# Kernel tuning notes

Measured on AMD Instinct MI355X. Metric: run time of the kernel, lower is better.

Reference implementation:

```python
import jax, jax.numpy as jnp
import numpy as np

B, S, D = 128, 256, 128
VOCAB, NH, K = 21, 4, 4
DI = 2 * D            # mLSTM inner dim (proj_factor=2)
QKB = 8               # qkv_proj_blocksize
NB = DI // QKB        # 32 block-diagonal qkv blocks
DHM = DI // NH        # 64 = mLSTM head dim
DHS = D // NH         # 32 = sLSTM head dim
FFU = 2 * D           # gated FFN up dim (proj_factor=2.0)


def _ln(x, w, eps=1e-5):
    mu = x.mean(-1, keepdims=True)
    var = x.var(-1, keepdims=True)
    return (x - mu) / jnp.sqrt(var + eps) * w


def _mh_ln(x, w, nh, eps=1e-5):
    # multi-head (group) layernorm: normalize each head's channels, scale by per-channel w
    b, s, d = x.shape
    xh = x.reshape(b, s, nh, d // nh)
    mu = xh.mean(-1, keepdims=True)
    var = xh.var(-1, keepdims=True)
    xn = (xh - mu) / jnp.sqrt(var + eps)
    return xn.reshape(b, s, d) * w


def _causal_conv(x, w, bias):
    # depthwise causal conv1d: x (B,S,C), w (C,K), left-pad K-1
    s = x.shape[1]
    k = w.shape[1]
    xp = jnp.pad(x, ((0, 0), (k - 1, 0), (0, 0)))
    return sum(xp[:, j:j + s, :] * w[:, j] for j in range(k)) + bias


def _blockdiag(x, w):
    # block-diagonal (headwise) linear: x (B,S,D), w (nb, out_per_block, in_per_block)
    b, s, d = x.shape
    nb = w.shape[0]
    xh = x.reshape(b, s, nb, d // nb)
    return jnp.einsum('bshd,hed->bshe', xh, w).reshape(b, s, -1)


def _mlstm_parallel(q, k, v, ip, fp, eps=1e-6):
    # parallel stabilized mLSTM; q,k,v (B,NH,S,DH); ip,fp (B,NH,S,1)
    b, nh, s, dh = q.shape
    log_f = jax.nn.log_sigmoid(fp)
    lf_cum = jnp.concatenate([jnp.zeros((b, nh, 1, 1), q.dtype),
                              jnp.cumsum(log_f, axis=2)], axis=2)      # (B,NH,S+1,1)
    m = lf_cum - jnp.swapaxes(lf_cum, -2, -1)                          # (B,NH,S+1,S+1)
    ltr = jnp.tril(jnp.ones((s, s), bool))
    log_fg = jnp.where(ltr, m[:, :, 1:, 1:], -jnp.inf)
    log_d = log_fg + jnp.swapaxes(ip, -2, -1)                          # (B,NH,S,S)
    max_d = jnp.max(log_d, axis=-1, keepdims=True)
    dmat = jnp.exp(log_d - max_d)
    qk = jnp.einsum('bhqd,bhkd->bhqk', q, k) / (dh ** 0.5)
    c = qk * dmat
    norm = jnp.maximum(jnp.abs(c.sum(-1, keepdims=True)), jnp.exp(-max_d))
    return jnp.einsum('bhqk,bhkd->bhqd', c / (norm + eps), v)


def _slstm_scan(gi, gf, gz, go, rec_w, bias):
    # sLSTM recurrence; g* (B,S,NH,DH); rec_w (NH,DH,4*DH); bias (NH,4*DH)
    b, s, nh, dh = gi.shape
    bi, bf, bz, bo = jnp.split(bias, 4, axis=-1)

    def step(carry, inp):
        h, c, n, m = carry
        ixt, fxt, zxt, oxt = inp
        rec = jnp.einsum('bhd,hde->bhe', h, rec_w)
        ri, rf, rz, ro = jnp.split(rec, 4, axis=-1)
        iraw = ixt + ri + bi
        fraw = fxt + rf + bf
        zraw = zxt + rz + bz
        oraw = oxt + ro + bo
        logfplusm = m + jax.nn.log_sigmoid(fraw)
        mnew = jnp.maximum(iraw, logfplusm)
        ig = jnp.exp(iraw - mnew)
        fg = jnp.exp(logfplusm - mnew)
        cnew = fg * c + ig * jnp.tanh(zraw)
        nnew = fg * n + ig
        hnew = jax.nn.sigmoid(oraw) * cnew / nnew
        return (hnew, cnew, nnew, mnew), hnew

    init = tuple(jnp.zeros((b, nh, dh), gi.dtype) for _ in range(4))
    xs = tuple(jnp.moveaxis(t, 1, 0) for t in (gi, gf, gz, go))
    _, ys = jax.lax.scan(step, init, xs)
    return jnp.moveaxis(ys, 0, 1)  # (B,S,NH,DH)


def _forward(x, emb, m_ln_w, m_up_w, m_conv_w, m_conv_b, m_q_w, m_k_w, m_v_w,
             m_ig_w, m_ig_b, m_fg_w, m_fg_b, m_on_w, m_skip, m_down_w,
             s_ln1_w, s_conv_w, s_conv_b, s_ig_w, s_fg_w, s_zg_w, s_og_w,
             s_rec_w, s_bias, s_gn_w, s_ln2_w, s_ff_up_w, s_ff_down_w,
             post_norm_w):
    h = emb[x]  # (B,S,D)
    # ---- block 0: mLSTM block (pre-LN residual) ----
    xn = _ln(h, m_ln_w)
    x_in, z = jnp.split(xn @ m_up_w.T, 2, axis=-1)          # each (B,S,DI)
    xca = jax.nn.silu(_causal_conv(x_in, m_conv_w, m_conv_b))
    q = _blockdiag(xca, m_q_w)
    kk = _blockdiag(xca, m_k_w)
    v = _blockdiag(x_in, m_v_w)
    ifin = jnp.concatenate([q, kk, v], axis=-1)             # (B,S,3*DI)
    ip = jnp.swapaxes(ifin @ m_ig_w.T + m_ig_b, 1, 2)[..., None]  # (B,NH,S,1)
    fp = jnp.swapaxes(ifin @ m_fg_w.T + m_fg_b, 1, 2)[..., None]
    to_heads = lambda t: jnp.swapaxes(t.reshape(B, S, NH, DHM), 1, 2)
    ht = _mlstm_parallel(to_heads(q), to_heads(kk), to_heads(v), ip, fp)
    hm = jnp.swapaxes(ht, 1, 2).reshape(B, S, DI)
    hm = _mh_ln(hm, m_on_w, NH)
    hm = (hm + m_skip * xca) * jax.nn.silu(z)
    h = h + hm @ m_down_w.T
    # ---- blocks 1,2: sLSTM blocks (pre-LN residual + gated gelu FFN) ----
    for i in range(2):
        xn = _ln(h, s_ln1_w[i])
        xc = jax.nn.silu(_causal_conv(xn, s_conv_w[i], s_conv_b[i]))
        gi = _blockdiag(xc, s_ig_w[i]).reshape(B, S, NH, DHS)
        gf = _blockdiag(xc, s_fg_w[i]).reshape(B, S, NH, DHS)
        gz = _blockdiag(xn, s_zg_w[i]).reshape(B, S, NH, DHS)
        go = _blockdiag(xn, s_og_w[i]).reshape(B, S, NH, DHS)
        y = _slstm_scan(gi, gf, gz, go, s_rec_w[i], s_bias[i])
        h = h + _mh_ln(y.reshape(B, S, D), s_gn_w[i], NH)
        xn2 = _ln(h, s_ln2_w[i])
        gate, up = jnp.split(xn2 @ s_ff_up_w[i].T, 2, axis=-1)
        h = h + (jax.nn.gelu(gate, approximate=False) * up) @ s_ff_down_w[i].T
    return _ln(h, post_norm_w)


def setup_inputs():
    key = jax.random.key(0)
    ks = iter(jax.random.split(key, 64))
    r = lambda shape, s=0.02: jax.random.normal(next(ks), shape, jnp.float32) * s
    inp = {}
    inp['x'] = jax.random.randint(next(ks), (B, S), 0, VOCAB)
    inp['emb'] = r((VOCAB, D)).at[0].set(0.0)  # padding_idx=0
    inp['m_ln_w'] = jnp.ones((D,), jnp.float32)
    inp['m_up_w'] = r((2 * DI, D))
    inp['m_conv_w'] = r((DI, K), 0.1)
    inp['m_conv_b'] = jnp.zeros((DI,), jnp.float32)
    inp['m_q_w'] = r((NB, QKB, QKB), 0.1)
    inp['m_k_w'] = r((NB, QKB, QKB), 0.1)
    inp['m_v_w'] = r((NB, QKB, QKB), 0.1)
    inp['m_ig_w'] = r((NH, 3 * DI))
    inp['m_ig_b'] = r((NH,), 0.1)
    inp['m_fg_w'] = r((NH, 3 * DI))
    inp['m_fg_b'] = jnp.linspace(3.0, 6.0, NH)  # forget-gate bias init
    inp['m_on_w'] = jnp.ones((DI,), jnp.float32)
    inp['m_skip'] = jnp.ones((DI,), jnp.float32)
    inp['m_down_w'] = r((D, DI))
    inp['s_ln1_w'] = jnp.ones((2, D), jnp.float32)
    inp['s_conv_w'] = r((2, D, K), 0.1)
    inp['s_conv_b'] = jnp.zeros((2, D), jnp.float32)
    inp['s_ig_w'] = r((2, NH, DHS, DHS), 0.05)
    inp['s_fg_w'] = r((2, NH, DHS, DHS), 0.05)
    inp['s_zg_w'] = r((2, NH, DHS, DHS), 0.05)
    inp['s_og_w'] = r((2, NH, DHS, DHS), 0.05)
    inp['s_rec_w'] = r((2, NH, DHS, 4 * DHS), 0.05)
    inp['s_bias'] = jnp.zeros((2, NH, 4 * DHS), jnp.float32).at[:, :, DHS:2 * DHS].set(jnp.linspace(3.0, 6.0, DHS))
    inp['s_gn_w'] = jnp.ones((2, D), jnp.float32)
    inp['s_ln2_w'] = jnp.ones((2, D), jnp.float32)
    inp['s_ff_up_w'] = r((2, 2 * FFU, D))
    inp['s_ff_down_w'] = r((2, D, FFU))
    inp['post_norm_w'] = jnp.ones((D,), jnp.float32)
    return inp


def reference(x, emb, m_ln_w, m_up_w, m_conv_w, m_conv_b, m_q_w, m_k_w, m_v_w,
              m_ig_w, m_ig_b, m_fg_w, m_fg_b, m_on_w, m_skip, m_down_w,
              s_ln1_w, s_conv_w, s_conv_b, s_ig_w, s_fg_w, s_zg_w, s_og_w,
              s_rec_w, s_bias, s_gn_w, s_ln2_w, s_ff_up_w, s_ff_down_w,
              post_norm_w):
    return _forward(x, emb, m_ln_w, m_up_w, m_conv_w, m_conv_b, m_q_w, m_k_w, m_v_w,
                    m_ig_w, m_ig_b, m_fg_w, m_fg_b, m_on_w, m_skip, m_down_w,
                    s_ln1_w, s_conv_w, s_conv_b, s_ig_w, s_fg_w, s_zg_w, s_og_w,
                    s_rec_w, s_bias, s_gn_w, s_ln2_w, s_ff_up_w, s_ff_down_w,
                    post_norm_w)
```

## Files before the change

### kernel.cpp

```cpp
#include <hip/hip_runtime.h>
#include <hip/hip_bf16.h>

#define BB 128
#define SS 256
#define DD 128
#define DI 256
#define NH 4
#define DHM 64
#define DHS 32
#define NROWS (BB*SS)

#define WAVE_SYNC() do { asm volatile("s_waitcnt lgkmcnt(0)" ::: "memory"); __builtin_amdgcn_wave_barrier(); } while (0)

typedef __attribute__((ext_vector_type(8))) short short8;
typedef __attribute__((ext_vector_type(4))) float f32x4;
typedef __attribute__((ext_vector_type(2))) int i32x2;

__device__ __forceinline__ float sigmoidf_(float x) { return 1.f / (1.f + __expf(-x)); }
__device__ __forceinline__ float siluf_(float x) { return x / (1.f + __expf(-x)); }
__device__ __forceinline__ float logsigf_(float x) {
    return (x >= 0.f) ? -log1pf(__expf(-x)) : x - log1pf(__expf(x));
}
__device__ __forceinline__ float geluf_(float g) {
    return 0.5f * g * (1.f + erff(g * 0.70710678118654752f));
}
__device__ __forceinline__ ushort bf16u(float x) {
    unsigned u = __float_as_uint(x);
    u += 0x7fffu + ((u >> 16) & 1u);
    return (ushort)(u >> 16);
}
__device__ __forceinline__ float ubf(ushort v) {
    return __uint_as_float((unsigned)v << 16);
}
__device__ __forceinline__ float rdlane(float v, int lane) {
    return __int_as_float(__builtin_amdgcn_readlane(__float_as_int(v), lane));
}
#define DPPADD(x, ctrl) ((x) + __int_as_float(__builtin_amdgcn_update_dpp(0, __float_as_int(x), (ctrl), 0xf, 0xf, true)))

__global__ __launch_bounds__(256) void tobf16_kernel(const float* __restrict__ src,
        ushort* __restrict__ dst, int n) {
    int i = blockIdx.x * 256 + threadIdx.x;
    if (i < n) dst[i] = bf16u(src[i]);
}

__global__ __launch_bounds__(256) void densify_kernel(const float* __restrict__ wi,
        const float* __restrict__ wf, const float* __restrict__ wz,
        const float* __restrict__ wo, ushort* __restrict__ dst) {
    int idx = blockIdx.x * 256 + threadIdx.x;
    int t = idx & 127;
    int oc = (idx >> 7) & 255;
    int pair = (idx >> 15) & 1;
    int i2 = idx >> 16;
    int h = oc >> 6, l = oc & 63, gate = (l >> 5) & 1, e = l & 31;
    const float* w = pair == 0 ? (gate == 0 ? wi : wf) : (gate == 0 ? wz : wo);
    float val = ((t >> 5) == h) ? w[i2 * 4096 + h * 1024 + e * 32 + (t & 31)] : 0.f;
    dst[idx] = bf16u(val);
}

__global__ __launch_bounds__(256) void densify_mgate_kernel(const float* __restrict__ igw,
        const float* __restrict__ fgw, ushort* __restrict__ dst) {
    int idx = blockIdx.x * 256 + threadIdx.x;
    if (idx >= 16 * 768) return;
    int t = idx % 768, j = idx / 768;
    float v = 0.f;
    if (j < 4) v = igw[j * 768 + t];
    else if (j < 8) v = fgw[(j - 4) * 768 + t];
    dst[idx] = bf16u(v);
}

__global__ __launch_bounds__(256) void embed_kernel(const int* __restrict__ x,
        const float* __restrict__ emb, float* __restrict__ h, int total) {
    int i = blockIdx.x * 256 + threadIdx.x;
    if (i >= total) return;
    int row = i >> 7;
    int c = i & 127;
    h[i] = emb[x[row] * DD + c];
}

__global__ __launch_bounds__(256) void ln128_kernel(const float* __restrict__ x,
        const float* __restrict__ w, float* __restrict__ out, ushort* __restrict__ outb) {
    int row = blockIdx.x * 4 + (threadIdx.x >> 6);
    int lane = threadIdx.x & 63;
    const float* xr = x + (size_t)row * DD;
    float a = xr[lane], b = xr[lane + 64];
    float s1 = a + b, s2 = a * a + b * b;
    #pragma unroll
    for (int o = 32; o; o >>= 1) { s1 += __shfl_xor(s1, o); s2 += __shfl_xor(s2, o); }
    float mu = s1 * (1.f / 128.f);
    float var = s2 * (1.f / 128.f) - mu * mu;
    float inv = rsqrtf(var + 1e-5f);
    float va = (a - mu) * inv * w[lane];
    float vb = (b - mu) * inv * w[lane + 64];
    if (out) {
        float* orow = out + (size_t)row * DD;
        orow[lane] = va; orow[lane + 64] = vb;
    }
    ushort* brow = outb + (size_t)row * DD;
    brow[lane] = bf16u(va); brow[lane + 64] = bf16u(vb);
}

__global__ __launch_bounds__(256, 2) void gemm_bf16_kernel(const ushort* __restrict__ A, int lda,
        const ushort* __restrict__ W, float* __restrict__ C, ushort* __restrict__ Cb,
        int ldc, int K, int addC) {
    __shared__ ushort As[128 * 32];
    __shared__ ushort Bs[128 * 32];
    int m0 = blockIdx.x * 128;
    int n0 = blockIdx.y * 128;
    int tid = threadIdx.x;
    int wv = tid >> 6, l = tid & 63;
    int lr = l & 15, lg = l >> 4, g4 = lg * 4;
    int wr = wv >> 1, wc = wv & 1;
    int sr = tid >> 1;
    int sc = (tid & 1) * 2;

    f32x4 acc[4][4] = {};
    for (int k0 = 0; k0 < K; k0 += 32) {
        __syncthreads();
        #pragma unroll
        for (int u = 0; u < 2; ++u) {
            int c = sc + u;
            uint4 av = *(const uint4*)(A + (size_t)(m0 + sr) * lda + k0 + c * 8);
            *(uint4*)(As + sr * 32 + ((c ^ (sr & 3)) * 8)) = av;
            uint4 wv4 = *(const uint4*)(W + (size_t)(n0 + sr) * K + k0 + c * 8);
            *(uint4*)(Bs + sr * 32 + ((c ^ (sr & 3)) * 8)) = wv4;
        }
        __syncthreads();
        short8 af[4], bf[4];
        #pragma unroll
        for (int fm = 0; fm < 4; ++fm) {
            int row = wr * 64 + fm * 16 + lr;
            af[fm] = *(const short8*)(As + row * 32 + ((lg ^ (row & 3)) * 8));
        }
        #pragma unroll
        for (int fn = 0; fn < 4; ++fn) {
            int row = wc * 64 + fn * 16 + lr;
            bf[fn] = *(const short8*)(Bs + row * 32 + ((lg ^ (row & 3)) * 8));
        }
        #pragma unroll
        for (int fm = 0; fm < 4; ++fm)
            #pragma unroll
            for (int fn = 0; fn < 4; ++fn)
                acc[fm][fn] = __builtin_amdgcn_mfma_f32_16x16x32_bf16(af[fm], bf[fn], acc[fm][fn], 0, 0, 0);
    }
    #pragma unroll
    for (int fm = 0; fm < 4; ++fm) {
        #pragma unroll
        for (int fn = 0; fn < 4; ++fn) {
            #pragma unroll
            for (int r = 0; r < 4; ++r) {
                size_t idx = (size_t)(m0 + wr * 64 + fm * 16 + g4 + r) * ldc + n0 + wc * 64 + fn * 16 + lr;
                if (Cb) Cb[idx] = bf16u(acc[fm][fn][r]);
                else if (addC) C[idx] += acc[fm][fn][r];
                else C[idx] = acc[fm][fn][r];
            }
        }
    }
}

__global__ __launch_bounds__(256, 2) void gemm_glu_kernel(const ushort* __restrict__ xzb,
        const ushort* __restrict__ W, float* __restrict__ C) {
    __shared__ ushort As[128 * 32];
    __shared__ ushort Bs[128 * 32];
    int m0 = blockIdx.x * 128;
    int tid = threadIdx.x;
    int wv = tid >> 6, l = tid & 63;
    int lr = l & 15, lg = l >> 4, g4 = lg * 4;
    int wr = wv >> 1, wc = wv & 1;
    int sr = tid >> 1;
    int sc = (tid & 1) * 2;

    f32x4 acc[4][4] = {};
    for (int k0 = 0; k0 < 256; k0 += 32) {
        __syncthreads();
        #pragma unroll
        for (int u = 0; u < 2; ++u) {
            int c = sc + u;
            short8 g8 = *(const short8*)(xzb + (size_t)(m0 + sr) * 512 + k0 + c * 8);
            short8 u8 = *(const short8*)(xzb + (size_t)(m0 + sr) * 512 + 256 + k0 + c * 8);
            short8 o8;
            #pragma unroll
            for (int t = 0; t < 8; ++t)
                o8[t] = (short)bf16u(geluf_(ubf((ushort)g8[t])) * ubf((ushort)u8[t]));
            *(short8*)(As + sr * 32 + ((c ^ (sr & 3)) * 8)) = o8;
            uint4 wv4 = *(const uint4*)(W + (size_t)sr * 256 + k0 + c * 8);
            *(uint4*)(Bs + sr * 32 + ((c ^ (sr & 3)) * 8)) = wv4;
        }
        __syncthreads();
        short8 af[4], bf[4];
        #pragma unroll
        for (int fm = 0; fm < 4; ++fm) {
            int row = wr * 64 + fm * 16 + lr;
            af[fm] = *(const short8*)(As + row * 32 + ((lg ^ (row & 3)) * 8));
        }
        #pragma unroll
        for (int fn = 0; fn < 4; ++fn) {
            int row = wc * 64 + fn * 16 + lr;
            bf[fn] = *(const short8*)(Bs + row * 32 + ((lg ^ (row & 3)) * 8));
        }
        #pragma unroll
        for (int fm = 0; fm < 4; ++fm)
            #pragma unroll
            for (int fn = 0; fn < 4; ++fn)
                acc[fm][fn] = __builtin_amdgcn_mfma_f32_16x16x32_bf16(af[fm], bf[fn], acc[fm][fn], 0, 0, 0);
    }
    #pragma unroll
    for (int fm = 0; fm < 4; ++fm) {
        #pragma unroll
        for (int fn = 0; fn < 4; ++fn) {
            #pragma unroll
            for (int r = 0; r < 4; ++r) {
                size_t idx = (size_t)(m0 + wr * 64 + fm * 16 + g4 + r) * 128 + wc * 64 + fn * 16 + lr;
                C[idx] += acc[fm][fn][r];
            }
        }
    }
}

__global__ __launch_bounds__(256) void gategemm_kernel(const ushort* __restrict__ qb,
        const ushort* __restrict__ kb, const ushort* __restrict__ vb,
        const ushort* __restrict__ W16, const float* __restrict__ igb,
        const float* __restrict__ fgb, float* __restrict__ ip, float* __restrict__ fp) {
    int tid = threadIdx.x;
    int wv = tid >> 6, l = tid & 63;
    int lr = l & 15, lg = l >> 4, g4 = lg * 4;
    int row0 = blockIdx.x * 128 + wv * 32;
    f32x4 acc[2] = {};
    #pragma unroll
    for (int k0 = 0; k0 < 768; k0 += 32) {
        short8 bfr = *(const short8*)(W16 + lr * 768 + k0 + lg * 8);
        #pragma unroll
        for (int mi = 0; mi < 2; ++mi) {
            int row = row0 + mi * 16 + lr;
            int b = row >> 8, s = row & 255;
            const ushort* src;
            size_t addr;
            if (k0 < 256) {
                src = qb;
                addr = ((size_t)(b * 4 + (k0 >> 6)) * 256 + s) * 64 + (k0 & 63) + lg * 8;
            } else if (k0 < 512) {
                int kq = k0 - 256;
                src = kb;
                addr = ((size_t)(b * 4 + (kq >> 6)) * 256 + s) * 64 + (kq & 63) + lg * 8;
            } else {
                src = vb;
                addr = (size_t)row * 256 + (k0 - 512) + lg * 8;
            }
            short8 afr = *(const short8*)(src + addr);
            acc[mi] = __builtin_amdgcn_mfma_f32_16x16x32_bf16(afr, bfr, acc[mi], 0, 0, 0);
        }
    }
    if (lr < 8) {
        float bias = (lr < 4) ? igb[lr] : fgb[lr - 4];
        float* dst = (lr < 4) ? ip : fp;
        int hh = lr & 3;
        #pragma unroll
        for (int mi = 0; mi < 2; ++mi) {
            #pragma unroll
            for (int r = 0; r < 4; ++r) {
                int row = row0 + mi * 16 + g4 + r;
                int b = row >> 8, s = row & 255;
                dst[(size_t)(b * 4 + hh) * 256 + s] = acc[mi][r] + bias;
            }
        }
    }
}

__global__ __launch_bounds__(256) void conv_silu_s_kernel(const ushort* __restrict__ xb,
        const float* __restrict__ w, const float* __restrict__ bias,
        ushort* __restrict__ outb, int total) {
    int i = blockIdx.x * 256 + threadIdx.x;
    if (i >= total) return;
    int c = i & 127;
    size_t row = (size_t)(i >> 7);
    int s = (int)(row & (SS - 1));
    float acc = bias[c];
    #pragma unroll
    for (int j = 0; j < 4; ++j) {
        int ss = s - 3 + j;
        if (ss >= 0) acc += ubf(xb[(row + (size_t)(j - 3)) * 128 + c]) * w[c * 4 + j];
    }
    outb[i] = bf16u(siluf_(acc));
}

__global__ __launch_bounds__(256) void mqkv_kernel(const ushort* __restrict__ xzb,
        const float* __restrict__ cw, const float* __restrict__ cb,
        const float* __restrict__ qw, const float* __restrict__ kw,
        const float* __restrict__ vw, ushort* __restrict__ xcab,
        ushort* __restrict__ qb16, ushort* __restrict__ kb16,
        ushort* __restrict__ vb16, int total) {
    int i = blockIdx.x * 256 + threadIdx.x;
    if (i >= total) return;
    int c = i & 255;
    size_t row = (size_t)(i >> 8);
    int nb = c >> 3, e = c & 7;
    int s = (int)(row & (SS - 1));
    float xin[4][8];
    #pragma unroll
    for (int j = 0; j < 4; ++j) {
        int ss = s - 3 + j;
        if (ss >= 0) {
            short8 v8 = *(const short8*)(xzb + (row + (size_t)(j - 3)) * 512 + nb * 8);
            #pragma unroll
            for (int t = 0; t < 8; ++t) xin[j][t] = ubf((ushort)v8[t]);
        } else {
            #pragma unroll
            for (int t = 0; t < 8; ++t) xin[j][t] = 0.f;
        }
    }
    float xc8[8];
    #pragma unroll
    for (int t = 0; t < 8; ++t) {
        int ch = nb * 8 + t;
        float acc = cb[ch];
        #pragma unroll
        for (int j = 0; j < 4; ++j) acc += xin[j][t] * cw[ch * 4 + j];
        xc8[t] = siluf_(acc);
    }
    const float* qw8 = qw + (size_t)(nb * 8 + e) * 8;
    const float* kw8 = kw + (size_t)(nb * 8 + e) * 8;
    const float* vw8 = vw + (size_t)(nb * 8 + e) * 8;
    float aq = 0.f, ak = 0.f, av = 0.f;
    #pragma unroll
    for (int t = 0; t < 8; ++t) {
        aq += xc8[t] * qw8[t];
        ak += xc8[t] * kw8[t];
        av += xin[3][t] * vw8[t];
    }
    xcab[row * 256 + c] = bf16u(xc8[e]);
    vb16[row * 256 + c] = bf16u(av);
    int h2 = c >> 6, dd = c & 63;
    size_t be = ((((row >> 8) << 2) + h2) * 256 + (row & 255)) * 64 + dd;
    qb16[be] = bf16u(aq);
    kb16[be] = bf16u(ak);
}

__global__ __launch_bounds__(64) void mprep_kernel(const float* __restrict__ ip,
        const float* __restrict__ fp, float* __restrict__ L,
        float* __restrict__ E, float* __restrict__ PM) {
    int bh = blockIdx.x;
    int lane = threadIdx.x;
    size_t base = (size_t)bh * SS + lane * 4;
    float lsv[4], ipv[4];
    #pragma unroll
    for (int u = 0; u < 4; ++u) {
        lsv[u] = logsigf_(fp[base + u]);
        ipv[u] = ip[base + u];
    }
    float p0 = lsv[0], p1 = p0 + lsv[1], p2 = p1 + lsv[2], p3 = p2 + lsv[3];
    float inc = p3;
    #pragma unroll
    for (int o = 1; o < 64; o <<= 1) {
        float wv = __shfl_up(inc, o);
        if (lane >= o) inc += wv;
    }
    float excl = inc - p3;
    float Lv[4] = {excl + p0, excl + p1, excl + p2, excl + p3};
    float Ev[4];
    #pragma unroll
    for (int u = 0; u < 4; ++u) Ev[u] = ipv[u] - Lv[u];
    float q0 = Ev[0], q1 = fmaxf(q0, Ev[1]), q2 = fmaxf(q1, Ev[2]), q3 = fmaxf(q2, Ev[3]);
    float incm = q3;
    #pragma unroll
    for (int o = 1; o < 64; o <<= 1) {
        float wv = __shfl_up(incm, o);
        if (lane >= o) incm = fmaxf(incm, wv);
    }
    float exm = __shfl_up(incm, 1);
    if (lane == 0) exm = -INFINITY;
    float qv[4] = {q0, q1, q2, q3};
    #pragma unroll
    for (int u = 0; u < 4; ++u) {
        L[base + u] = Lv[u];
        E[base + u] = Ev[u];
        PM[base + u] = fmaxf(exm, qv[u]);
    }
}

__global__ __launch_bounds__(256) void vtrans_kernel(const ushort* __restrict__ vb,
        ushort* __restrict__ vt) {
    int blk = blockIdx.x;
    int st = blk & 3, bh = blk >> 2;
    int b = bh >> 2, h = bh & 3;
    int tid = threadIdx.x;
    __shared__ ushort tile[64][68];
    int s0 = st * 64;
    #pragma unroll
    for (int u = 0; u < 16; ++u) {
        int idx = u * 256 + tid;
        int sl = idx >> 6, dl = idx & 63;
        tile[sl][dl] = vb[((size_t)(b * 256 + s0 + sl)) * 256 + h * 64 + dl];
    }
    __syncthreads();
    #pragma unroll
    for (int u = 0; u < 16; ++u) {
        int idx = u * 256 + tid;
        int dl = idx >> 6, sl = idx & 63;
        vt[((size_t)bh * 64 + dl) * 256 + s0 + sl] = tile[sl][dl];
    }
}

__global__ __launch_bounds__(256, 2) void mlstm_mfma_kernel(
        const ushort* __restrict__ qb, const ushort* __restrict__ kb,
        const ushort* __restrict__ vt, const float* __restrict__ Lg,
        const float* __restrict__ Eg, const float* __restrict__ PMg,
        float* __restrict__ hmout) {
    int bh = blockIdx.x;
    int b = bh >> 2, h = bh & 3;
    int tid = threadIdx.x;
    int wv = tid >> 6, l = tid & 63;
    int lr = l & 15, lg = l >> 4, g4 = lg * 4;

    __shared__ ushort Kb[16384];
    __shared__ ushort Vt[16384];
    __shared__ ushort Pl[4 * 640];
    __shared__ float sE[SS], sPM[SS], sL[SS];

    const size_t gb16 = (size_t)bh * 16384;
    #pragma unroll
    for (int p2 = 0; p2 < 8; ++p2) {
        int id = p2 * 256 + tid;
        int r = id >> 3, c = id & 7;
        uint4 kval = *(const uint4*)(kb + gb16 + r * 64 + c * 8);
        *(uint4*)(Kb + r * 64 + ((c ^ (r & 7)) * 8)) = kval;
        int d = id >> 5, c2 = id & 31;
        uint4 vval = *(const uint4*)(vt + gb16 + d * 256 + c2 * 8);
        *(uint4*)(Vt + d * 256 + ((c2 ^ (d & 7)) * 8)) = vval;
    }
    sE[tid]  = Eg[(size_t)bh * SS + tid];
    sPM[tid] = PMg[(size_t)bh * SS + tid];
    sL[tid]  = Lg[(size_t)bh * SS + tid];
    __syncthreads();

    f32x4 O[4][4] = {};
    float csum[4][4] = {};
    const int pmap[4] = {wv, 7 - wv, 8 + wv, 15 - wv};
    ushort* Pw = Pl + wv * 640;
    size_t obase = (size_t)(b * SS) * 256 + h * 64;

    #pragma unroll
    for (int rf = 0; rf < 4; ++rf) {
        int p = pmap[rf];
        int r0 = p * 16;
        short8 qf0 = *(const short8*)(qb + gb16 + (r0 + lr) * 64 + lg * 8);
        short8 qf1 = *(const short8*)(qb + gb16 + (r0 + lr) * 64 + 32 + lg * 8);
        float pmv[4], lv[4];
        #pragma unroll
        for (int r = 0; r < 4; ++r) { pmv[r] = sPM[r0 + g4 + r]; lv[r] = sL[r0 + g4 + r]; }
        int jtmax = r0 >> 5;
        #pragma unroll 1
        for (int jt = 0; jt <= jtmax; ++jt) {
            int jb = jt * 32;
            f32x4 s0 = {0.f, 0.f, 0.f, 0.f}, s1 = {0.f, 0.f, 0.f, 0.f};
            {
                int j = jb + lr;
                int sw = j & 7;
                short8 k00 = *(const short8*)(Kb + j * 64 + ((lg)     ^ sw) * 8);
                short8 k01 = *(const short8*)(Kb + j * 64 + ((4 + lg) ^ sw) * 8);
                int j2 = jb + 16 + lr;
                int sw2 = j2 & 7;
                short8 k10 = *(const short8*)(Kb + j2 * 64 + ((lg)     ^ sw2) * 8);
                short8 k11 = *(const short8*)(Kb + j2 * 64 + ((4 + lg) ^ sw2) * 8);
                s0 = __builtin_amdgcn_mfma_f32_16x16x32_bf16(qf0, k00, s0, 0, 0, 0);
                s0 = __builtin_amdgcn_mfma_f32_16x16x32_bf16(qf1, k01, s0, 0, 0, 0);
                s1 = __builtin_amdgcn_mfma_f32_16x16x32_bf16(qf0, k10, s1, 0, 0, 0);
                s1 = __builtin_amdgcn_mfma_f32_16x16x32_bf16(qf1, k11, s1, 0, 0, 0);
            }
            float e0 = sE[jb + lr], e1 = sE[jb + 16 + lr];
            int j0 = jb + lr, j1 = jb + 16 + lr;
            #pragma unroll
            for (int r = 0; r < 4; ++r) {
                int i = r0 + g4 + r;
                float sc0 = (j0 <= i) ? s0[r] * 0.125f * __expf(e0 - pmv[r]) : 0.f;
                float sc1 = (j1 <= i) ? s1[r] * 0.125f * __expf(e1 - pmv[r]) : 0.f;
                csum[rf][r] += sc0 + sc1;
                Pw[(g4 + r) * 40 + lr] = bf16u(sc0);
                Pw[(g4 + r) * 40 + 16 + lr] = bf16u(sc1);
            }
            WAVE_SYNC();
            short8 pf = *(const short8*)(Pw + lr * 40 + lg * 8);
            #pragma unroll
            for (int dc = 0; dc < 4; ++dc) {
                int d = dc * 16 + lr;
                int chunk = (jt * 4 + lg) ^ (d & 7);
                short8 vf = *(const short8*)(Vt + d * 256 + chunk * 8);
                O[rf][dc] = __builtin_amdgcn_mfma_f32_16x16x32_bf16(pf, vf, O[rf][dc], 0, 0, 0);
            }
        }
        float rinv[4];
        #pragma unroll
        for (int r = 0; r < 4; ++r) {
            float cs = csum[rf][r];
            cs += __shfl_xor(cs, 1); cs += __shfl_xor(cs, 2);
            cs += __shfl_xor(cs, 4); cs += __shfl_xor(cs, 8);
            float nrm = fmaxf(fabsf(cs), __expf(-(lv[r] + pmv[r]))) + 1e-6f;
            rinv[r] = 1.f / nrm;
        }
        #pragma unroll
        for (int dc = 0; dc < 4; ++dc)
            #pragma unroll
            for (int r = 0; r < 4; ++r)
                hmout[obase + (size_t)(r0 + g4 + r) * 256 + dc * 16 + lr] = O[rf][dc][r] * rinv[r];
    }
}

__global__ __launch_bounds__(256) void mpost_kernel(const float* __restrict__ hm,
        const ushort* __restrict__ xzb, const ushort* __restrict__ xcab,
        const float* __restrict__ onw, const float* __restrict__ skip,
        ushort* __restrict__ outb) {
    int row = blockIdx.x;
    int t = threadIdx.x;
    float hv = hm[(size_t)row * 256 + t];
    float s1 = hv, s2 = hv * hv;
    #pragma unroll
    for (int o = 32; o; o >>= 1) { s1 += __shfl_xor(s1, o); s2 += __shfl_xor(s2, o); }
    float mu = s1 * (1.f / 64.f);
    float var = s2 * (1.f / 64.f) - mu * mu;
    float xnv = (hv - mu) * rsqrtf(var + 1e-5f) * onw[t];
    float z = ubf(xzb[(size_t)row * 512 + 256 + t]);
    float val = (xnv + skip[t] * ubf(xcab[(size_t)row * 256 + t])) * siluf_(z);
    outb[(size_t)row * 256 + t] = bf16u(val);
}

__global__ __launch_bounds__(64, 1) void slstm_scan_kernel(const ushort* __restrict__ gifb,
        const ushort* __restrict__ gzob, const float* __restrict__ rec_w,
        const float* __restrict__ bias, const float* __restrict__ gnw,
        float* __restrict__ hbuf) {
    int bh = blockIdx.x;
    int b = bh >> 2, h = bh & 3;
    int l = threadIdx.x;
    int c = l & 31;
    bool lo = (l < 32);
    unsigned wpk[32];
    const float* wp = rec_w + (size_t)h * 4096 + l;
    #pragma unroll
    for (int d = 0; d < 32; ++d) {
        float w0v = wp[d * 128];
        float w1v = wp[d * 128 + 64];
        wpk[d] = ((unsigned)bf16u(w1v) << 16) | (unsigned)bf16u(w0v);
    }
    float b0 = bias[h * 128 + l];
    float b1 = bias[h * 128 + 64 + l];
    float gw = gnw[h * 32 + c];
    float cst = 0.f, nst = 0.f, hreg = 0.f;
    size_t gb = (size_t)b * SS * 256 + h * 64 + l;
    size_t hb = (size_t)b * SS * 128 + h * 32 + c;
    float pg0[4], pg1[4], ph[4];
    #pragma unroll
    for (int u = 0; u < 4; ++u) {
        pg0[u] = ubf(gifb[gb + (size_t)u * 256]);
        pg1[u] = ubf(gzob[gb + (size_t)u * 256]);
        ph[u]  = hbuf[hb + (size_t)u * 128];
    }
    for (int s = 0; s < SS; s += 4) {
        #pragma unroll
        for (int u = 0; u < 4; ++u) {
            float a00 = 0.f, a01 = 0.f, a02 = 0.f, a03 = 0.f;
            float a10 = 0.f, a11 = 0.f, a12 = 0.f, a13 = 0.f;
            #pragma unroll
            for (int d = 0; d < 32; d += 4) {
                float h0 = rdlane(hreg, d);
                float h1 = rdlane(hreg, d + 1);
                float h2 = rdlane(hreg, d + 2);
                float h3 = rdlane(hreg, d + 3);
                unsigned p0 = wpk[d], p1 = wpk[d + 1], p2 = wpk[d + 2], p3 = wpk[d + 3];
                a00 += __uint_as_float(p0 << 16) * h0;
                a10 += __uint_as_float(p0) * h0;
                a01 += __uint_as_float(p1 << 16) * h1;
                a11 += __uint_as_float(p1) * h1;
                a02 += __uint_as_float(p2 << 16) * h2;
                a12 += __uint_as_float(p2) * h2;
                a03 += __uint_as_float(p3 << 16) * h3;
                a13 += __uint_as_float(p3) * h3;
            }
            float raw0 = pg0[u] + ((a00 + a01) + (a02 + a03)) + b0;
            float raw1 = pg1[u] + ((a10 + a11) + (a12 + a13)) + b1;
            float hcur = ph[u];
            int s4 = s + 4 + u;
            if (s4 < SS) {
                pg0[u] = ubf(gifb[gb + (size_t)s4 * 256]);
                pg1[u] = ubf(gzob[gb + (size_t)s4 * 256]);
                ph[u]  = hbuf[hb + (size_t)s4 * 128];
            }
            i32x2 r0p = __builtin_amdgcn_permlane32_swap(__float_as_int(raw0), __float_as_int(raw0), false, false);
            i32x2 r1p = __builtin_amdgcn_permlane32_swap(__float_as_int(raw1), __float_as_int(raw1), false, false);
            float q0 = __int_as_float(lo ? r0p.y : r0p.x);
            float q1 = __int_as_float(lo ? r1p.y : r1p.x);
            float iraw = lo ? raw0 : q0;
            float zraw = lo ? raw1 : q1;
            float fraw = lo ? q0 : raw0;
            float oraw = lo ? q1 : raw1;
            float fg = __builtin_amdgcn_rcpf(1.f + __expf(-fraw));
            float ig = __expf(iraw);
            float e2z = __expf(2.f * zraw);
            float tz = 1.f - 2.f * __builtin_amdgcn_rcpf(e2z + 1.f);
            cst = fg * cst + ig * tz;
            nst = fg * nst + ig;
            float sg = __builtin_amdgcn_rcpf(1.f + __expf(-oraw));
            float hv = sg * cst * __builtin_amdgcn_rcpf(nst);
            hreg = hv;
            float s1 = hv, s2 = hv * hv;
            s1 = DPPADD(s1, 0x111); s2 = DPPADD(s2, 0x111);
            s1 = DPPADD(s1, 0x112); s2 = DPPADD(s2, 0x112);
            s1 = DPPADD(s1, 0x114); s2 = DPPADD(s2, 0x114);
            s1 = DPPADD(s1, 0x118); s2 = DPPADD(s2, 0x118);
            s1 = DPPADD(s1, 0x142); s2 = DPPADD(s2, 0x142);
            s1 = DPPADD(s1, 0x143); s2 = DPPADD(s2, 0x143);
            float mu = rdlane(s1, 63) * (1.f / 64.f);
            float var = rdlane(s2, 63) * (1.f / 64.f) - mu * mu;
            float outv = (hv - mu) * rsqrtf(var + 1e-5f) * gw;
            if (lo) hbuf[hb + (size_t)(s + u) * 128] = hcur + outv;
        }
    }
}

extern "C" void kernel_launch(void* const* d_in, const int* in_sizes, int n_in,
                              void* d_out, int out_size, void* d_ws, size_t ws_size,
                              hipStream_t stream) {
    const int*   x        = (const int*)d_in[0];
    const float* emb      = (const float*)d_in[1];
    const float* m_ln_w   = (const float*)d_in[2];
    const float* m_up_w   = (const float*)d_in[3];
    const float* m_conv_w = (const float*)d_in[4];
    const float* m_conv_b = (const float*)d_in[5];
    const float* m_q_w    = (const float*)d_in[6];
    const float* m_k_w    = (const float*)d_in[7];
    const float* m_v_w    = (const float*)d_in[8];
    const float* m_ig_w   = (const float*)d_in[9];
    const float* m_ig_b   = (const float*)d_in[10];
    const float* m_fg_w   = (const float*)d_in[11];
    const float* m_fg_b   = (const float*)d_in[12];
    const float* m_on_w   = (const float*)d_in[13];
    const float* m_skip   = (const float*)d_in[14];
    const float* m_down_w = (const float*)d_in[15];
    const float* s_ln1_w  = (const float*)d_in[16];
    const float* s_conv_w = (const float*)d_in[17];
    const float* s_conv_b = (const float*)d_in[18];
    const float* s_ig_w   = (const float*)d_in[19];
    const float* s_fg_w   = (const float*)d_in[20];
    const float* s_zg_w   = (const float*)d_in[21];
    const float* s_og_w   = (const float*)d_in[22];
    const float* s_rec_w  = (const float*)d_in[23];
    const float* s_bias   = (const float*)d_in[24];
    const float* s_gn_w   = (const float*)d_in[25];
    const float* s_ln2_w  = (const float*)d_in[26];
    const float* s_ff_up_w   = (const float*)d_in[27];
    const float* s_ff_down_w = (const float*)d_in[28];
    const float* post_norm_w = (const float*)d_in[29];
    float* out = (float*)d_out;

    float* ws = (float*)d_ws;
    const size_t NR = NROWS;
    float* h   = ws;
    float* hm  = h   + NR * 128;
    float* regA = hm  + NR * 256;
    float* regB = regA + NR * 128;
    float* gip = regB + NR * 128;
    float* gfp = gip + 512 * 256;
    float* gL  = gfp + 512 * 256;
    float* gE  = gL  + 512 * 256;
    float* gPM = gE  + 512 * 256;
    float* extra = gPM + 512 * 256;
    ushort* xnb   = (ushort*)extra;
    ushort* xzb   = xnb + NR * 128;
    ushort* xcab  = xzb + NR * 512;
    ushort* qb16  = xcab + NR * 256;
    ushort* vb16  = qb16 + NR * 256;
    ushort* upb   = vb16 + NR * 256;
    ushort* downb = upb + 512 * 128;
    ushort* ffupb = downb + 128 * 256;
    ushort* ffdownb = ffupb + 2 * 512 * 128;
    ushort* sgwb  = ffdownb + 2 * 128 * 256;
    ushort* w16b  = sgwb + 2 * 2 * 256 * 128;
    ushort* kb16   = (ushort*)out;
    ushort* vtb    = (ushort*)regA;
    ushort* gifb   = (ushort*)regA;
    ushort* mpostb = (ushort*)regB;
    ushort* gzob   = (ushort*)regB;
    ushort* xcb    = qb16;

    tobf16_kernel<<<(512 * 128 + 255) / 256, 256, 0, stream>>>(m_up_w, upb, 512 * 128);
    tobf16_kernel<<<(128 * 256 + 255) / 256, 256, 0, stream>>>(m_down_w, downb, 128 * 256);
    tobf16_kernel<<<(2 * 512 * 128 + 255) / 256, 256, 0, stream>>>(s_ff_up_w, ffupb, 2 * 512 * 128);
    tobf16_kernel<<<(2 * 128 * 256 + 255) / 256, 256, 0, stream>>>(s_ff_down_w, ffdownb, 2 * 128 * 256);
    densify_kernel<<<(2 * 2 * 256 * 128) / 256, 256, 0, stream>>>(s_ig_w, s_fg_w, s_zg_w, s_og_w, sgwb);
    densify_mgate_kernel<<<(16 * 768 + 255) / 256, 256, 0, stream>>>(m_ig_w, m_fg_w, w16b);

    embed_kernel<<<(NR * 128) / 256, 256, 0, stream>>>(x, emb, h, NR * 128);
    ln128_kernel<<<NR / 4, 256, 0, stream>>>(h, m_ln_w, nullptr, xnb);
    gemm_bf16_kernel<<<dim3(NR / 128, 4), 256, 0, stream>>>(xnb, 128, upb, nullptr, xzb, 512, 128, 0);
    mqkv_kernel<<<(NR * 256) / 256, 256, 0, stream>>>(xzb, m_conv_w, m_conv_b,
            m_q_w, m_k_w, m_v_w, xcab, qb16, kb16, vb16, NR * 256);
    gategemm_kernel<<<NR / 128, 256, 0, stream>>>(qb16, kb16, vb16, w16b, m_ig_b, m_fg_b, gip, gfp);
    mprep_kernel<<<BB * NH, 64, 0, stream>>>(gip, gfp, gL, gE, gPM);
    vtrans_kernel<<<BB * NH * 4, 256, 0, stream>>>(vb16, vtb);
    mlstm_mfma_kernel<<<BB * NH, 256, 0, stream>>>(qb16, kb16, vtb, gL, gE, gPM, hm);
    mpost_kernel<<<NR, 256, 0, stream>>>(hm, xzb, xcab, m_on_w, m_skip, mpostb);
    gemm_bf16_kernel<<<dim3(NR / 128, 1), 256, 0, stream>>>(mpostb, 256, downb, h, nullptr, 128, 256, 1);

    for (int i2 = 0; i2 < 2; ++i2) {
        ln128_kernel<<<NR / 4, 256, 0, stream>>>(h, s_ln1_w + i2 * 128, nullptr, xnb);
        conv_silu_s_kernel<<<(NR * 128) / 256, 256, 0, stream>>>(xnb, s_conv_w + i2 * 128 * 4,
                s_conv_b + i2 * 128, xcb, NR * 128);
        gemm_bf16_kernel<<<dim3(NR / 128, 2), 256, 0, stream>>>(xcb, 128, sgwb + (size_t)(i2 * 2 + 0) * 256 * 128, nullptr, gifb, 256, 128, 0);
        gemm_bf16_kernel<<<dim3(NR / 128, 2), 256, 0, stream>>>(xnb, 128, sgwb + (size_t)(i2 * 2 + 1) * 256 * 128, nullptr, gzob, 256, 128, 0);
        slstm_scan_kernel<<<BB * NH, 64, 0, stream>>>(gifb, gzob,
                s_rec_w + i2 * 4 * 32 * 128, s_bias + i2 * 4 * 128, s_gn_w + i2 * 128, h);
        ln128_kernel<<<NR / 4, 256, 0, stream>>>(h, s_ln2_w + i2 * 128, nullptr, xnb);
        gemm_bf16_kernel<<<dim3(NR / 128, 4), 256, 0, stream>>>(xnb, 128, ffupb + (size_t)i2 * 512 * 128, nullptr, xzb, 512, 128, 0);
        gemm_glu_kernel<<<NR / 128, 256, 0, stream>>>(xzb, ffdownb + (size_t)i2 * 128 * 256, h);
    }
    ln128_kernel<<<NR / 4, 256, 0, stream>>>(h, post_norm_w, out, xnb);
}
```

Baseline: 726.7 us.

## Fuse weight prep, embed+LN, mLSTM post-norm, sLSTM gate GEMMs, defer scan norm

Six weight-conversion launches are merged into one kernel, and embedding lookup is fused with the first layernorm. The mLSTM output normalization, skip and gating are folded into the attention kernel, so the fp32 hm buffer no longer round-trips through memory. The two sLSTM gate GEMMs become one launch, and the sLSTM scan defers each step's group-norm reduction and store into the next step to overlap it with the recurrence. The final layernorm no longer writes an unused bf16 copy. The mLSTM epilogue now issues strided, less coalesced bf16 loads and stores from inside the attention kernel.

```diff
diff --git a/kernel.cpp b/kernel.cpp
--- a/kernel.cpp
+++ b/kernel.cpp
@@ -37,44 +37,65 @@
 }
 #define DPPADD(x, ctrl) ((x) + __int_as_float(__builtin_amdgcn_update_dpp(0, __float_as_int(x), (ctrl), 0xf, 0xf, true)))
 
-__global__ __launch_bounds__(256) void tobf16_kernel(const float* __restrict__ src,
-        ushort* __restrict__ dst, int n) {
-    int i = blockIdx.x * 256 + threadIdx.x;
-    if (i < n) dst[i] = bf16u(src[i]);
-}
-
-__global__ __launch_bounds__(256) void densify_kernel(const float* __restrict__ wi,
+__global__ __launch_bounds__(256) void wprep_kernel(const float* __restrict__ m_up_w,
+        const float* __restrict__ m_down_w, const float* __restrict__ s_ff_up_w,
+        const float* __restrict__ s_ff_down_w, const float* __restrict__ wi,
         const float* __restrict__ wf, const float* __restrict__ wz,
-        const float* __restrict__ wo, ushort* __restrict__ dst) {
-    int idx = blockIdx.x * 256 + threadIdx.x;
-    int t = idx & 127;
-    int oc = (idx >> 7) & 255;
-    int pair = (idx >> 15) & 1;
-    int i2 = idx >> 16;
-    int h = oc >> 6, l = oc & 63, gate = (l >> 5) & 1, e = l & 31;
-    const float* w = pair == 0 ? (gate == 0 ? wi : wf) : (gate == 0 ? wz : wo);
-    float val = ((t >> 5) == h) ? w[i2 * 4096 + h * 1024 + e * 32 + (t & 31)] : 0.f;
-    dst[idx] = bf16u(val);
-}
-
-__global__ __launch_bounds__(256) void densify_mgate_kernel(const float* __restrict__ igw,
-        const float* __restrict__ fgw, ushort* __restrict__ dst) {
-    int idx = blockIdx.x * 256 + threadIdx.x;
-    if (idx >= 16 * 768) return;
-    int t = idx % 768, j = idx / 768;
-    float v = 0.f;
-    if (j < 4) v = igw[j * 768 + t];
-    else if (j < 8) v = fgw[(j - 4) * 768 + t];
-    dst[idx] = bf16u(v);
-}
-
-__global__ __launch_bounds__(256) void embed_kernel(const int* __restrict__ x,
-        const float* __restrict__ emb, float* __restrict__ h, int total) {
-    int i = blockIdx.x * 256 + threadIdx.x;
-    if (i >= total) return;
-    int row = i >> 7;
-    int c = i & 127;
-    h[i] = emb[x[row] * DD + c];
+        const float* __restrict__ wo, const float* __restrict__ igw,
+        const float* __restrict__ fgw,
+        ushort* __restrict__ upb, ushort* __restrict__ downb,
+        ushort* __restrict__ ffupb, ushort* __restrict__ ffdownb,
+        ushort* __restrict__ sgwb, ushort* __restrict__ w16b) {
+    int gid = blockIdx.x * 256 + threadIdx.x;
+    if (gid < 65536) {
+        upb[gid] = bf16u(m_up_w[gid]);
+    } else if (gid < 98304) {
+        int i = gid - 65536;
+        downb[i] = bf16u(m_down_w[i]);
+    } else if (gid < 229376) {
+        int i = gid - 98304;
+        ffupb[i] = bf16u(s_ff_up_w[i]);
+    } else if (gid < 294912) {
+        int i = gid - 229376;
+        ffdownb[i] = bf16u(s_ff_down_w[i]);
+    } else if (gid < 557056) {
+        int idx = gid - 294912;
+        int t = idx & 127;
+        int oc = (idx >> 7) & 255;
+        int pair = (idx >> 15) & 1;
+        int i2 = idx >> 16;
+        int h = oc >> 6, l = oc & 63, gate = (l >> 5) & 1, e = l & 31;
+        const float* w = pair == 0 ? (gate == 0 ? wi : wf) : (gate == 0 ? wz : wo);
+        float val = ((t >> 5) == h) ? w[i2 * 4096 + h * 1024 + e * 32 + (t & 31)] : 0.f;
+        sgwb[idx] = bf16u(val);
+    } else if (gid < 569344) {
+        int idx = gid - 557056;
+        int t = idx % 768, j = idx / 768;
+        float v = 0.f;
+        if (j < 4) v = igw[j * 768 + t];
+        else if (j < 8) v = fgw[(j - 4) * 768 + t];
+        w16b[idx] = bf16u(v);
+    }
+}
+
+__global__ __launch_bounds__(256) void embed_ln_kernel(const int* __restrict__ x,
+        const float* __restrict__ emb, const float* __restrict__ w,
+        float* __restrict__ h, ushort* __restrict__ outb) {
+    int row = blockIdx.x * 4 + (threadIdx.x >> 6);
+    int lane = threadIdx.x & 63;
+    int tok = x[row];
+    float a = emb[tok * DD + lane], b = emb[tok * DD + 64 + lane];
+    h[(size_t)row * DD + lane] = a;
+    h[(size_t)row * DD + 64 + lane] = b;
+    float s1 = a + b, s2 = a * a + b * b;
+    #pragma unroll
+    for (int o = 32; o; o >>= 1) { s1 += __shfl_xor(s1, o); s2 += __shfl_xor(s2, o); }
+    float mu = s1 * (1.f / 128.f);
+    float var = s2 * (1.f / 128.f) - mu * mu;
+    float inv = rsqrtf(var + 1e-5f);
+    ushort* brow = outb + (size_t)row * DD;
+    brow[lane] = bf16u((a - mu) * inv * w[lane]);
+    brow[lane + 64] = bf16u((b - mu) * inv * w[lane + 64]);
 }
 
 __global__ __launch_bounds__(256) void ln128_kernel(const float* __restrict__ x,
@@ -95,8 +116,10 @@
         float* orow = out + (size_t)row * DD;
         orow[lane] = va; orow[lane + 64] = vb;
     }
-    ushort* brow = outb + (size_t)row * DD;
-    brow[lane] = bf16u(va); brow[lane + 64] = bf16u(vb);
+    if (outb) {
+        ushort* brow = outb + (size_t)row * DD;
+        brow[lane] = bf16u(va); brow[lane + 64] = bf16u(vb);
+    }
 }
 
 __global__ __launch_bounds__(256, 2) void gemm_bf16_kernel(const ushort* __restrict__ A, int lda,
@@ -157,6 +180,64 @@
     }
 }
 
+__global__ __launch_bounds__(256, 2) void sgate_gemm_kernel(const ushort* __restrict__ xcb,
+        const ushort* __restrict__ xnb, const ushort* __restrict__ Wif,
+        const ushort* __restrict__ Wzo, ushort* __restrict__ gifb, ushort* __restrict__ gzob) {
+    __shared__ ushort As[128 * 32];
+    __shared__ ushort Bs[128 * 32];
+    int y = blockIdx.y;
+    const ushort* A = (y < 2) ? xcb : xnb;
+    const ushort* W = (y < 2) ? Wif : Wzo;
+    ushort* Cb = (y < 2) ? gifb : gzob;
+    int m0 = blockIdx.x * 128;
+    int n0 = (y & 1) * 128;
+    int tid = threadIdx.x;
+    int wv = tid >> 6, l = tid & 63;
+    int lr = l & 15, lg = l >> 4, g4 = lg * 4;
+    int wr = wv >> 1, wc = wv & 1;
+    int sr = tid >> 1;
+    int sc = (tid & 1) * 2;
+
+    f32x4 acc[4][4] = {};
+    for (int k0 = 0; k0 < 128; k0 += 32) {
+        __syncthreads();
+        #pragma unroll
+        for (int u = 0; u < 2; ++u) {
+            int c = sc + u;
+            uint4 av = *(const uint4*)(A + (size_t)(m0 + sr) * 128 + k0 + c * 8);
+            *(uint4*)(As + sr * 32 + ((c ^ (sr & 3)) * 8)) = av;
+            uint4 wv4 = *(const uint4*)(W + (size_t)(n0 + sr) * 128 + k0 + c * 8);
+            *(uint4*)(Bs + sr * 32 + ((c ^ (sr & 3)) * 8)) = wv4;
+        }
+        __syncthreads();
+        short8 af[4], bf[4];
+        #pragma unroll
+        for (int fm = 0; fm < 4; ++fm) {
+            int row = wr * 64 + fm * 16 + lr;
+            af[fm] = *(const short8*)(As + row * 32 + ((lg ^ (row & 3)) * 8));
+        }
+        #pragma unroll
+        for (int fn = 0; fn < 4; ++fn) {
+            int row = wc * 64 + fn * 16 + lr;
+            bf[fn] = *(const short8*)(Bs + row * 32 + ((lg ^ (row & 3)) * 8));
+        }
+        #pragma unroll
+        for (int fm = 0; fm < 4; ++fm)
+            #pragma unroll
+            for (int fn = 0; fn < 4; ++fn)
+                acc[fm][fn] = __builtin_amdgcn_mfma_f32_16x16x32_bf16(af[fm], bf[fn], acc[fm][fn], 0, 0, 0);
+    }
+    #pragma unroll
+    for (int fm = 0; fm < 4; ++fm)
+        #pragma unroll
+        for (int fn = 0; fn < 4; ++fn)
+            #pragma unroll
+            for (int r = 0; r < 4; ++r) {
+                size_t idx = (size_t)(m0 + wr * 64 + fm * 16 + g4 + r) * 256 + n0 + wc * 64 + fn * 16 + lr;
+                Cb[idx] = bf16u(acc[fm][fn][r]);
+            }
+}
+
 __global__ __launch_bounds__(256, 2) void gemm_glu_kernel(const ushort* __restrict__ xzb,
         const ushort* __restrict__ W, float* __restrict__ C) {
     __shared__ ushort As[128 * 32];
@@ -204,16 +285,14 @@
                 acc[fm][fn] = __builtin_amdgcn_mfma_f32_16x16x32_bf16(af[fm], bf[fn], acc[fm][fn], 0, 0, 0);
     }
     #pragma unroll
-    for (int fm = 0; fm < 4; ++fm) {
-        #pragma unroll
-        for (int fn = 0; fn < 4; ++fn) {
+    for (int fm = 0; fm < 4; ++fm)
+        #pragma unroll
+        for (int fn = 0; fn < 4; ++fn)
             #pragma unroll
             for (int r = 0; r < 4; ++r) {
                 size_t idx = (size_t)(m0 + wr * 64 + fm * 16 + g4 + r) * 128 + wc * 64 + fn * 16 + lr;
                 C[idx] += acc[fm][fn][r];
             }
-        }
-    }
 }
 
 __global__ __launch_bounds__(256) void gategemm_kernel(const ushort* __restrict__ qb,
@@ -403,7 +482,9 @@
         const ushort* __restrict__ qb, const ushort* __restrict__ kb,
         const ushort* __restrict__ vt, const float* __restrict__ Lg,
         const float* __restrict__ Eg, const float* __restrict__ PMg,
-        float* __restrict__ hmout) {
+        const ushort* __restrict__ xzb, const ushort* __restrict__ xcab,
+        const float* __restrict__ onw, const float* __restrict__ skip,
+        ushort* __restrict__ outb) {
     int bh = blockIdx.x;
     int b = bh >> 2, h = bh & 3;
     int tid = threadIdx.x;
@@ -431,11 +512,18 @@
     sL[tid]  = Lg[(size_t)bh * SS + tid];
     __syncthreads();
 
+    float onwv[4], skipv[4];
+    #pragma unroll
+    for (int dc = 0; dc < 4; ++dc) {
+        int ch = h * 64 + dc * 16 + lr;
+        onwv[dc] = onw[ch];
+        skipv[dc] = skip[ch];
+    }
+
     f32x4 O[4][4] = {};
     float csum[4][4] = {};
     const int pmap[4] = {wv, 7 - wv, 8 + wv, 15 - wv};
     ushort* Pw = Pl + wv * 640;
-    size_t obase = (size_t)(b * SS) * 256 + h * 64;
 
     #pragma unroll
     for (int rf = 0; rf < 4; ++rf) {
@@ -486,39 +574,36 @@
                 O[rf][dc] = __builtin_amdgcn_mfma_f32_16x16x32_bf16(pf, vf, O[rf][dc], 0, 0, 0);
             }
         }
-        float rinv[4];
         #pragma unroll
         for (int r = 0; r < 4; ++r) {
             float cs = csum[rf][r];
             cs += __shfl_xor(cs, 1); cs += __shfl_xor(cs, 2);
             cs += __shfl_xor(cs, 4); cs += __shfl_xor(cs, 8);
             float nrm = fmaxf(fabsf(cs), __expf(-(lv[r] + pmv[r]))) + 1e-6f;
-            rinv[r] = 1.f / nrm;
-        }
-        #pragma unroll
-        for (int dc = 0; dc < 4; ++dc)
-            #pragma unroll
-            for (int r = 0; r < 4; ++r)
-                hmout[obase + (size_t)(r0 + g4 + r) * 256 + dc * 16 + lr] = O[rf][dc][r] * rinv[r];
-    }
-}
-
-__global__ __launch_bounds__(256) void mpost_kernel(const float* __restrict__ hm,
-        const ushort* __restrict__ xzb, const ushort* __restrict__ xcab,
-        const float* __restrict__ onw, const float* __restrict__ skip,
-        ushort* __restrict__ outb) {
-    int row = blockIdx.x;
-    int t = threadIdx.x;
-    float hv = hm[(size_t)row * 256 + t];
-    float s1 = hv, s2 = hv * hv;
-    #pragma unroll
-    for (int o = 32; o; o >>= 1) { s1 += __shfl_xor(s1, o); s2 += __shfl_xor(s2, o); }
-    float mu = s1 * (1.f / 64.f);
-    float var = s2 * (1.f / 64.f) - mu * mu;
-    float xnv = (hv - mu) * rsqrtf(var + 1e-5f) * onw[t];
-    float z = ubf(xzb[(size_t)row * 512 + 256 + t]);
-    float val = (xnv + skip[t] * ubf(xcab[(size_t)row * 256 + t])) * siluf_(z);
-    outb[(size_t)row * 256 + t] = bf16u(val);
+            float rinv = 1.f / nrm;
+            float v0 = O[rf][0][r] * rinv, v1 = O[rf][1][r] * rinv;
+            float v2 = O[rf][2][r] * rinv, v3 = O[rf][3][r] * rinv;
+            float s1m = v0 + v1 + v2 + v3;
+            float s2m = v0 * v0 + v1 * v1 + v2 * v2 + v3 * v3;
+            s1m += __shfl_xor(s1m, 1); s2m += __shfl_xor(s2m, 1);
+            s1m += __shfl_xor(s1m, 2); s2m += __shfl_xor(s2m, 2);
+            s1m += __shfl_xor(s1m, 4); s2m += __shfl_xor(s2m, 4);
+            s1m += __shfl_xor(s1m, 8); s2m += __shfl_xor(s2m, 8);
+            float mu = s1m * (1.f / 64.f);
+            float var = s2m * (1.f / 64.f) - mu * mu;
+            float inv = rsqrtf(var + 1e-5f);
+            int grow = b * 256 + r0 + g4 + r;
+            float vv[4] = {v0, v1, v2, v3};
+            #pragma unroll
+            for (int dc = 0; dc < 4; ++dc) {
+                int ch = h * 64 + dc * 16 + lr;
+                float z = ubf(xzb[(size_t)grow * 512 + 256 + ch]);
+                float xnv = (vv[dc] - mu) * inv * onwv[dc];
+                float val = (xnv + skipv[dc] * ubf(xcab[(size_t)grow * 256 + ch])) * siluf_(z);
+                outb[(size_t)grow * 256 + ch] = bf16u(val);
+            }
+        }
+    }
 }
 
 __global__ __launch_bounds__(64, 1) void slstm_scan_kernel(const ushort* __restrict__ gifb,
@@ -551,6 +636,8 @@
         pg1[u] = ubf(gzob[gb + (size_t)u * 256]);
         ph[u]  = hbuf[hb + (size_t)u * 128];
     }
+    float pend_hv = 0.f, pend_hcur = 0.f;
+    int pend_off = 0;
     for (int s = 0; s < SS; s += 4) {
         #pragma unroll
         for (int u = 0; u < 4; ++u) {
@@ -575,6 +662,19 @@
             float raw0 = pg0[u] + ((a00 + a01) + (a02 + a03)) + b0;
             float raw1 = pg1[u] + ((a10 + a11) + (a12 + a13)) + b1;
             float hcur = ph[u];
+            {
+                float s1 = pend_hv, s2 = pend_hv * pend_hv;
+                s1 = DPPADD(s1, 0x111); s2 = DPPADD(s2, 0x111);
+                s1 = DPPADD(s1, 0x112); s2 = DPPADD(s2, 0x112);
+                s1 = DPPADD(s1, 0x114); s2 = DPPADD(s2, 0x114);
+                s1 = DPPADD(s1, 0x118); s2 = DPPADD(s2, 0x118);
+                s1 = DPPADD(s1, 0x142); s2 = DPPADD(s2, 0x142);
+                s1 = DPPADD(s1, 0x143); s2 = DPPADD(s2, 0x143);
+                float mu = rdlane(s1, 63) * (1.f / 64.f);
+                float var = rdlane(s2, 63) * (1.f / 64.f) - mu * mu;
+                float outv = (pend_hv - mu) * rsqrtf(var + 1e-5f) * gw;
+                if (lo) hbuf[hb + (size_t)pend_off * 128] = pend_hcur + outv;
+            }
             int s4 = s + 4 + u;
             if (s4 < SS) {
                 pg0[u] = ubf(gifb[gb + (size_t)s4 * 256]);
@@ -598,18 +698,23 @@
             float sg = __builtin_amdgcn_rcpf(1.f + __expf(-oraw));
             float hv = sg * cst * __builtin_amdgcn_rcpf(nst);
             hreg = hv;
-            float s1 = hv, s2 = hv * hv;
-            s1 = DPPADD(s1, 0x111); s2 = DPPADD(s2, 0x111);
-            s1 = DPPADD(s1, 0x112); s2 = DPPADD(s2, 0x112);
-            s1 = DPPADD(s1, 0x114); s2 = DPPADD(s2, 0x114);
-            s1 = DPPADD(s1, 0x118); s2 = DPPADD(s2, 0x118);
-            s1 = DPPADD(s1, 0x142); s2 = DPPADD(s2, 0x142);
-            s1 = DPPADD(s1, 0x143); s2 = DPPADD(s2, 0x143);
-            float mu = rdlane(s1, 63) * (1.f / 64.f);
-            float var = rdlane(s2, 63) * (1.f / 64.f) - mu * mu;
-            float outv = (hv - mu) * rsqrtf(var + 1e-5f) * gw;
-            if (lo) hbuf[hb + (size_t)(s + u) * 128] = hcur + outv;
-        }
+            pend_hv = hv;
+            pend_hcur = hcur;
+            pend_off = s + u;
+        }
+    }
+    {
+        float s1 = pend_hv, s2 = pend_hv * pend_hv;
+        s1 = DPPADD(s1, 0x111); s2 = DPPADD(s2, 0x111);
+        s1 = DPPADD(s1, 0x112); s2 = DPPADD(s2, 0x112);
+        s1 = DPPADD(s1, 0x114); s2 = DPPADD(s2, 0x114);
+        s1 = DPPADD(s1, 0x118); s2 = DPPADD(s2, 0x118);
+        s1 = DPPADD(s1, 0x142); s2 = DPPADD(s2, 0x142);
+        s1 = DPPADD(s1, 0x143); s2 = DPPADD(s2, 0x143);
+        float mu = rdlane(s1, 63) * (1.f / 64.f);
+        float var = rdlane(s2, 63) * (1.f / 64.f) - mu * mu;
+        float outv = (pend_hv - mu) * rsqrtf(var + 1e-5f) * gw;
+        if (lo) hbuf[hb + (size_t)pend_off * 128] = pend_hcur + outv;
     }
 }
 
@@ -651,8 +756,7 @@
     float* ws = (float*)d_ws;
     const size_t NR = NROWS;
     float* h   = ws;
-    float* hm  = h   + NR * 128;
-    float* regA = hm  + NR * 256;
+    float* regA = h   + NR * 128;
     float* regB = regA + NR * 128;
     float* gip = regB + NR * 128;
     float* gfp = gip + 512 * 256;
@@ -678,36 +782,33 @@
     ushort* gzob   = (ushort*)regB;
     ushort* xcb    = qb16;
 
-    tobf16_kernel<<<(512 * 128 + 255) / 256, 256, 0, stream>>>(m_up_w, upb, 512 * 128);
-    tobf16_kernel<<<(128 * 256 + 255) / 256, 256, 0, stream>>>(m_down_w, downb, 128 * 256);
-    tobf16_kernel<<<(2 * 512 * 128 + 255) / 256, 256, 0, stream>>>(s_ff_up_w, ffupb, 2 * 512 * 128);
-    tobf16_kernel<<<(2 * 128 * 256 + 255) / 256, 256, 0, stream>>>(s_ff_down_w, ffdownb, 2 * 128 * 256);
-    densify_kernel<<<(2 * 2 * 256 * 128) / 256, 256, 0, stream>>>(s_ig_w, s_fg_w, s_zg_w, s_og_w, sgwb);
-    densify_mgate_kernel<<<(16 * 768 + 255) / 256, 256, 0, stream>>>(m_ig_w, m_fg_w, w16b);
-
-    embed_kernel<<<(NR * 128) / 256, 256, 0, stream>>>(x, emb, h, NR * 128);
-    ln128_kernel<<<NR / 4, 256, 0, stream>>>(h, m_ln_w, nullptr, xnb);
+    wprep_kernel<<<(569344 + 255) / 256, 256, 0, stream>>>(m_up_w, m_down_w, s_ff_up_w,
+            s_ff_down_w, s_ig_w, s_fg_w, s_zg_w, s_og_w, m_ig_w, m_fg_w,
+            upb, downb, ffupb, ffdownb, sgwb, w16b);
+
+    embed_ln_kernel<<<NR / 4, 256, 0, stream>>>(x, emb, m_ln_w, h, xnb);
     gemm_bf16_kernel<<<dim3(NR / 128, 4), 256, 0, stream>>>(xnb, 128, upb, nullptr, xzb, 512, 128, 0);
     mqkv_kernel<<<(NR * 256) / 256, 256, 0, stream>>>(xzb, m_conv_w, m_conv_b,
             m_q_w, m_k_w, m_v_w, xcab, qb16, kb16, vb16, NR * 256);
     gategemm_kernel<<<NR / 128, 256, 0, stream>>>(qb16, kb16, vb16, w16b, m_ig_b, m_fg_b, gip, gfp);
     mprep_kernel<<<BB * NH, 64, 0, stream>>>(gip, gfp, gL, gE, gPM);
     vtrans_kernel<<<BB * NH * 4, 256, 0, stream>>>(vb16, vtb);
-    mlstm_mfma_kernel<<<BB * NH, 256, 0, stream>>>(qb16, kb16, vtb, gL, gE, gPM, hm);
-    mpost_kernel<<<NR, 256, 0, stream>>>(hm, xzb, xcab, m_on_w, m_skip, mpostb);
+    mlstm_mfma_kernel<<<BB * NH, 256, 0, stream>>>(qb16, kb16, vtb, gL, gE, gPM,
+            xzb, xcab, m_on_w, m_skip, mpostb);
     gemm_bf16_kernel<<<dim3(NR / 128, 1), 256, 0, stream>>>(mpostb, 256, downb, h, nullptr, 128, 256, 1);
 
     for (int i2 = 0; i2 < 2; ++i2) {
         ln128_kernel<<<NR / 4, 256, 0, stream>>>(h, s_ln1_w + i2 * 128, nullptr, xnb);
         conv_silu_s_kernel<<<(NR * 128) / 256, 256, 0, stream>>>(xnb, s_conv_w + i2 * 128 * 4,
                 s_conv_b + i2 * 128, xcb, NR * 128);
-        gemm_bf16_kernel<<<dim3(NR / 128, 2), 256, 0, stream>>>(xcb, 128, sgwb + (size_t)(i2 * 2 + 0) * 256 * 128, nullptr, gifb, 256, 128, 0);
-        gemm_bf16_kernel<<<dim3(NR / 128, 2), 256, 0, stream>>>(xnb, 128, sgwb + (size_t)(i2 * 2 + 1) * 256 * 128, nullptr, gzob, 256, 128, 0);
+        sgate_gemm_kernel<<<dim3(NR / 128, 4), 256, 0, stream>>>(xcb, xnb,
+                sgwb + (size_t)(i2 * 2 + 0) * 256 * 128, sgwb + (size_t)(i2 * 2 + 1) * 256 * 128,
+                gifb, gzob);
         slstm_scan_kernel<<<BB * NH, 64, 0, stream>>>(gifb, gzob,
                 s_rec_w + i2 * 4 * 32 * 128, s_bias + i2 * 4 * 128, s_gn_w + i2 * 128, h);
         ln128_kernel<<<NR / 4, 256, 0, stream>>>(h, s_ln2_w + i2 * 128, nullptr, xnb);
         gemm_bf16_kernel<<<dim3(NR / 128, 4), 256, 0, stream>>>(xnb, 128, ffupb + (size_t)i2 * 512 * 128, nullptr, xzb, 512, 128, 0);
         gemm_glu_kernel<<<NR / 128, 256, 0, stream>>>(xzb, ffdownb + (size_t)i2 * 128 * 256, h);
     }
-    ln128_kernel<<<NR / 4, 256, 0, stream>>>(h, post_norm_w, out, xnb);
-}
+    ln128_kernel<<<NR / 4, 256, 0, stream>>>(h, post_norm_w, out, nullptr);
+}
```

Result: faster. 685.7 us (-5.6%).
